# Performance work log

Hardware: AMD Instinct MI355X
Metric: run time of the kernel (lower is better)

Reference implementation:

```python
import jax, jax.numpy as jnp
import numpy as np

D_IN = 1024
D_OUT = 1024
SEQ = 2048
BATCH = 4


def setup_inputs() -> dict:
    key = jax.random.key(0)
    kx, kq, kk, kv = jax.random.split(key, 4)
    x = jax.random.normal(kx, (BATCH, SEQ, D_IN), dtype=jnp.float32)
    s = 1.0 / np.sqrt(D_IN)
    Wq = jax.random.uniform(kq, (D_IN, D_OUT), dtype=jnp.float32, minval=-s, maxval=s)
    Wk = jax.random.uniform(kk, (D_IN, D_OUT), dtype=jnp.float32, minval=-s, maxval=s)
    Wv = jax.random.uniform(kv, (D_IN, D_OUT), dtype=jnp.float32, minval=-s, maxval=s)
    return {"x": x, "Wq": Wq, "Wk": Wk, "Wv": Wv}


def reference(x, Wq, Wk, Wv):
    d_k = Wq.shape[1]
    q = jnp.einsum('bsd,de->bse', x, Wq)
    k = jnp.einsum('bsd,de->bse', x, Wk)
    v = jnp.einsum('bsd,de->bse', x, Wv)
    # [B, S, S] raw scores
    scores = jnp.einsum('bqe,bke->bqk', q, k)
    S = scores.shape[-1]
    causal = jnp.triu(jnp.ones((S, S), dtype=bool), k=1)  # True above diagonal
    scores = jnp.where(causal, -jnp.inf, scores)
    attn = jax.nn.softmax(scores * (d_k ** -0.5), axis=-1)
    # dropout p=0.0 -> identity
    return jnp.einsum('bqk,bke->bqe', attn, v)
```

## Files before the change

kernel.cpp:

```cpp
#include <hip/hip_runtime.h>
#include <hip/hip_bf16.h>

typedef unsigned short u16;
typedef __bf16 bfx8 __attribute__((ext_vector_type(8)));
typedef float fx4 __attribute__((ext_vector_type(4)));

#define SEQ 2048
#define DIM 1024
#define NBATCH 4
#define SCALE 0.03125f
#define NEL ((size_t)NBATCH * SEQ * DIM)

__device__ inline u16 f2bf(float f) {
    __bf16 h = (__bf16)f;
    return __builtin_bit_cast(unsigned short, h);
}

#define GLL(gp, lp) __builtin_amdgcn_global_load_lds( \
    (const __attribute__((address_space(1))) unsigned int*)(gp), \
    (__attribute__((address_space(3))) unsigned int*)(lp), 16, 0, 0)

__global__ __launch_bounds__(256) void prep(
    const float* __restrict__ X,
    const float* __restrict__ Wq, const float* __restrict__ Wk,
    const float* __restrict__ Wv,
    u16* __restrict__ XB, u16* __restrict__ WB, u16* __restrict__ WTv,
    float* __restrict__ Lrow)
{
    __shared__ u16 t[32][33];
    int bid = blockIdx.x;
    int tid = threadIdx.x;
    if (bid < 8192) {
        size_t i = (size_t)bid * 256 + tid;
        float4 v = ((const float4*)X)[i];
        uint2 pk;
        pk.x = (unsigned)f2bf(v.x) | ((unsigned)f2bf(v.y) << 16);
        pk.y = (unsigned)f2bf(v.z) | ((unsigned)f2bf(v.w) << 16);
        ((uint2*)XB)[i] = pk;
    } else if (bid < 10240) {
        int b2 = bid - 8192;
        const float* W = (b2 < 1024) ? Wq : Wk;
        u16* out = WB + (size_t)(b2 >> 10) * 1024 * 1024;
        size_t i = (size_t)(b2 & 1023) * 256 + tid;
        float4 v = ((const float4*)W)[i];
        uint2 pk;
        pk.x = (unsigned)f2bf(v.x) | ((unsigned)f2bf(v.y) << 16);
        pk.y = (unsigned)f2bf(v.z) | ((unsigned)f2bf(v.w) << 16);
        ((uint2*)out)[i] = pk;
    } else if (bid < 11264) {
        int t2 = bid - 10240;
        int n0 = (t2 & 31) * 32, k0 = (t2 >> 5) * 32;
        int tx = tid & 31, ty = tid >> 5;
        #pragma unroll
        for (int i = 0; i < 32; i += 8)
            t[ty + i][tx] = f2bf(Wv[(size_t)(k0 + ty + i) * 1024 + n0 + tx]);
        __syncthreads();
        #pragma unroll
        for (int i = 0; i < 32; i += 8)
            WTv[(size_t)(n0 + ty + i) * 1024 + k0 + tx] = t[tx][ty + i];
    } else {
        int i = (bid - 11264) * 256 + tid;
        Lrow[i] = 0.0f;
    }
}

__global__ __launch_bounds__(256) void gemm_m(
    const u16* __restrict__ WBk, const u16* __restrict__ WBq, u16* __restrict__ MT)
{
    int m0 = blockIdx.y * 128, n0 = blockIdx.x * 128;
    __shared__ __align__(16) u16 As[128 * 32];
    __shared__ __align__(16) u16 Bs[128 * 32];
    int tid = threadIdx.x, lane = tid & 63, w = tid >> 6;
    int wm = w >> 1, wn = w & 1, lo = lane & 15, qd = lane >> 4;
    fx4 acc[4][4] = {};

    int c0 = tid, c1 = tid + 256;
    const u16* a0 = WBk + (size_t)(m0 + (c0 >> 2)) * 1024 + (((c0 & 3) ^ ((c0 >> 2) & 3)) * 8);
    const u16* a1 = WBk + (size_t)(m0 + (c1 >> 2)) * 1024 + (((c1 & 3) ^ ((c1 >> 2) & 3)) * 8);
    const u16* b0 = WBq + (size_t)(n0 + (c0 >> 2)) * 1024 + (((c0 & 3) ^ ((c0 >> 2) & 3)) * 8);
    const u16* b1 = WBq + (size_t)(n0 + (c1 >> 2)) * 1024 + (((c1 & 3) ^ ((c1 >> 2) & 3)) * 8);

    int sw = (qd ^ (lo & 3)) * 8;
    for (int k0 = 0; k0 < 1024; k0 += 32) {
        GLL(a0 + k0, &As[(size_t)c0 * 8]);
        GLL(a1 + k0, &As[(size_t)c1 * 8]);
        GLL(b0 + k0, &Bs[(size_t)c0 * 8]);
        GLL(b1 + k0, &Bs[(size_t)c1 * 8]);
        __syncthreads();
        bfx8 af[4], bf[4];
        #pragma unroll
        for (int i = 0; i < 4; i++)
            af[i] = *(const bfx8*)(&As[(wm * 64 + i * 16 + lo) * 32 + sw]);
        #pragma unroll
        for (int j = 0; j < 4; j++)
            bf[j] = *(const bfx8*)(&Bs[(wn * 64 + j * 16 + lo) * 32 + sw]);
        #pragma unroll
        for (int i = 0; i < 4; i++)
            #pragma unroll
            for (int j = 0; j < 4; j++)
                acc[i][j] = __builtin_amdgcn_mfma_f32_16x16x32_bf16(af[i], bf[j], acc[i][j], 0, 0, 0);
        __syncthreads();
    }
    #pragma unroll
    for (int i = 0; i < 4; i++)
        #pragma unroll
        for (int j = 0; j < 4; j++)
            #pragma unroll
            for (int r = 0; r < 4; r++)
                MT[(size_t)(m0 + wm * 64 + i * 16 + qd * 4 + r) * 1024
                   + n0 + wn * 64 + j * 16 + lo] = f2bf(acc[i][j][r]);
}

__global__ __launch_bounds__(512) void gemm256(
    const u16* __restrict__ XB, const u16* __restrict__ MT,
    const u16* __restrict__ WTv,
    u16* __restrict__ Yo, u16* __restrict__ VTo)
{
    const int work = ((blockIdx.x & 7) << 5) + ((int)blockIdx.x >> 3);
    const int z = work >> 7;
    const int m0 = ((work >> 2) & 31) * 256;
    const int n0 = (work & 3) * 256;
    const u16* Bop = (z == 0) ? MT : WTv;

    __shared__ __align__(16) u16 SM[65536];

    const int tid = threadIdx.x, lane = tid & 63, w = tid >> 6;
    const int wm = w >> 2, wn = w & 3, lo = lane & 15, qd = lane >> 4;
    const int swl = lo & 7;

    fx4 acc[8][4] = {};

    const u16* sA[4]; const u16* sB[4]; int dofs[4];
    #pragma unroll
    for (int p = 0; p < 4; ++p) {
        int n = p * 512 + tid;
        int row = n >> 3;
        int c = (n & 7) ^ (row & 7);
        sA[p] = XB  + (size_t)(m0 + row) * 1024 + c * 8;
        sB[p] = Bop + (size_t)(n0 + row) * 1024 + c * 8;
        dofs[p] = n * 8;
    }

    auto stage = [&](int kt2) {
        const int bb = (kt2 & 1) * 16384;
        #pragma unroll
        for (int p = 0; p < 4; ++p) GLL(sA[p] + kt2 * 64, &SM[bb + dofs[p]]);
        #pragma unroll
        for (int p = 0; p < 4; ++p) GLL(sB[p] + kt2 * 64, &SM[32768 + bb + dofs[p]]);
    };

    stage(0);
    stage(1);
    asm volatile("s_waitcnt vmcnt(8)" ::: "memory");
    __builtin_amdgcn_s_barrier();
    asm volatile("" ::: "memory");

    bfx8 af[4][2], bfA[2][2], bfB[2][2];

    for (int kt = 0; kt < 16; ++kt) {
        const u16* Ab = SM + (kt & 1) * 16384;
        const u16* Bb = SM + 32768 + (kt & 1) * 16384;

        #pragma unroll
        for (int ph = 0; ph < 4; ++ph) {
            const int mh = ph >> 1, nh = ph & 1;
            if (nh == 0) {
                #pragma unroll
                for (int ii = 0; ii < 4; ++ii)
                    #pragma unroll
                    for (int ks = 0; ks < 2; ++ks)
                        af[ii][ks] = *(const bfx8*)(Ab
                            + (wm * 128 + (mh * 4 + ii) * 16 + lo) * 64
                            + ((ks * 4 + qd) ^ swl) * 8);
            }
            if (ph == 0) {
                #pragma unroll
                for (int jn = 0; jn < 2; ++jn)
                    #pragma unroll
                    for (int ks = 0; ks < 2; ++ks)
                        bfA[jn][ks] = *(const bfx8*)(Bb
                            + (wn * 64 + jn * 16 + lo) * 64
                            + ((ks * 4 + qd) ^ swl) * 8);
            }
            if (ph == 1) {
                #pragma unroll
                for (int jn = 0; jn < 2; ++jn)
                    #pragma unroll
                    for (int ks = 0; ks < 2; ++ks)
                        bfB[jn][ks] = *(const bfx8*)(Bb
                            + (wn * 64 + (2 + jn) * 16 + lo) * 64
                            + ((ks * 4 + qd) ^ swl) * 8);
            }
            __builtin_amdgcn_s_barrier();
            asm volatile("s_waitcnt lgkmcnt(0)" ::: "memory");
            __builtin_amdgcn_sched_barrier(0);
            __builtin_amdgcn_s_setprio(1);
            #pragma unroll
            for (int ii = 0; ii < 4; ++ii)
                #pragma unroll
                for (int jn = 0; jn < 2; ++jn)
                    #pragma unroll
                    for (int ks = 0; ks < 2; ++ks) {
                        if (nh == 0)
                            acc[mh * 4 + ii][jn] = __builtin_amdgcn_mfma_f32_16x16x32_bf16(
                                af[ii][ks], bfA[jn][ks], acc[mh * 4 + ii][jn], 0, 0, 0);
                        else
                            acc[mh * 4 + ii][2 + jn] = __builtin_amdgcn_mfma_f32_16x16x32_bf16(
                                af[ii][ks], bfB[jn][ks], acc[mh * 4 + ii][2 + jn], 0, 0, 0);
                    }
            __builtin_amdgcn_s_setprio(0);
            __builtin_amdgcn_s_barrier();
            asm volatile("" ::: "memory");
        }
        if (kt < 14) stage(kt + 2);
        if (kt < 15) {
            if (kt < 14) asm volatile("s_waitcnt vmcnt(8)" ::: "memory");
            else         asm volatile("s_waitcnt vmcnt(0)" ::: "memory");
            __builtin_amdgcn_s_barrier();
            asm volatile("" ::: "memory");
        }
    }

    if (z == 0) {
        #pragma unroll
        for (int i = 0; i < 8; i++)
            #pragma unroll
            for (int j = 0; j < 4; j++)
                #pragma unroll
                for (int r = 0; r < 4; r++) {
                    int row = m0 + wm * 128 + i * 16 + qd * 4 + r;
                    int col = n0 + wn * 64 + j * 16 + lo;
                    Yo[(size_t)row * 1024 + col] = f2bf(acc[i][j][r]);
                }
    } else {
        u16 (*Ct)[258] = (u16(*)[258])SM;
        const int bb = m0 >> 11;
        const int sbase = m0 & 2047;
        #pragma unroll
        for (int half = 0; half < 2; ++half) {
            __syncthreads();
            if (wm == half) {
                #pragma unroll
                for (int i = 0; i < 8; i++)
                    #pragma unroll
                    for (int j = 0; j < 4; j++)
                        #pragma unroll
                        for (int r = 0; r < 4; r++)
                            Ct[i * 16 + qd * 4 + r][wn * 64 + j * 16 + lo] = f2bf(acc[i][j][r]);
            }
            __syncthreads();
            for (int e = tid; e < 16384; e += 512) {
                int d = e >> 6, s2 = (e & 63) * 2;
                unsigned pk = (unsigned)Ct[s2][d] | ((unsigned)Ct[s2 + 1][d] << 16);
                *(unsigned*)&VTo[((size_t)bb * DIM + (n0 + d)) * SEQ
                                 + sbase + half * 128 + s2] = pk;
            }
        }
    }
}

__global__ __launch_bounds__(512) void sgemm_exp(
    const u16* __restrict__ Y, const u16* __restrict__ XB,
    u16* __restrict__ P, float* __restrict__ Lrow)
{
    const int k = blockIdx.x;
    const int work = (k & 7) * 68 + (k >> 3);
    const int b = work / 136;
    const int t = work % 136;
    int i = (int)((sqrtf(8.0f * t + 1.0f) - 1.0f) * 0.5f);
    while ((i + 1) * (i + 2) / 2 <= t) i++;
    while (i * (i + 1) / 2 > t) i--;
    int j = t - i * (i + 1) / 2;

    const u16* Yb = Y + (size_t)b * SEQ * DIM;
    const u16* Xb = XB + (size_t)b * SEQ * DIM;
    u16* Pb = P + (size_t)b * SEQ * SEQ;
    float* Lb = Lrow + (size_t)b * SEQ;

    int m0 = i * 128, n0 = j * 128;

    __shared__ __align__(16) u16 SM[32768];

    int tid = threadIdx.x, lane = tid & 63, w = tid >> 6;
    int wm = w >> 2, wn = w & 3, lo = lane & 15, qd = lane >> 4;
    int swl = lo & 7;

    fx4 acc[4][2] = {};

    int c0 = tid, c1 = tid + 512;
    const u16* a0 = Yb + (size_t)(m0 + (c0 >> 3)) * 1024 + (((c0 & 7) ^ ((c0 >> 3) & 7)) * 8);
    const u16* a1 = Yb + (size_t)(m0 + (c1 >> 3)) * 1024 + (((c1 & 7) ^ ((c1 >> 3) & 7)) * 8);
    const u16* b0 = Xb + (size_t)(n0 + (c0 >> 3)) * 1024 + (((c0 & 7) ^ ((c0 >> 3) & 7)) * 8);
    const u16* b1 = Xb + (size_t)(n0 + (c1 >> 3)) * 1024 + (((c1 & 7) ^ ((c1 >> 3) & 7)) * 8);
    int d0 = c0 * 8, d1 = c1 * 8;

    auto stage = [&](int kt2) {
        int bb = (kt2 & 1) * 8192;
        GLL(a0 + kt2 * 64, &SM[bb + d0]);
        GLL(a1 + kt2 * 64, &SM[bb + d1]);
        GLL(b0 + kt2 * 64, &SM[16384 + bb + d0]);
        GLL(b1 + kt2 * 64, &SM[16384 + bb + d1]);
    };

    stage(0);
    stage(1);
    asm volatile("s_waitcnt vmcnt(4)" ::: "memory");
    __builtin_amdgcn_s_barrier();
    asm volatile("" ::: "memory");

    for (int kt = 0; kt < 16; ++kt) {
        const u16* Ab = SM + (kt & 1) * 8192;
        const u16* Bb = SM + 16384 + (kt & 1) * 8192;

        #pragma unroll
        for (int kc = 0; kc < 2; ++kc) {
            bfx8 af[4], bf[2];
            int sw = ((kc * 4 + qd) ^ swl) * 8;
            #pragma unroll
            for (int ii = 0; ii < 4; ++ii)
                af[ii] = *(const bfx8*)(Ab + (wm * 64 + ii * 16 + lo) * 64 + sw);
            #pragma unroll
            for (int jn = 0; jn < 2; ++jn)
                bf[jn] = *(const bfx8*)(Bb + (wn * 32 + jn * 16 + lo) * 64 + sw);
            __builtin_amdgcn_s_barrier();
            asm volatile("s_waitcnt lgkmcnt(0)" ::: "memory");
            __builtin_amdgcn_sched_barrier(0);
            __builtin_amdgcn_s_setprio(1);
            #pragma unroll
            for (int ii = 0; ii < 4; ++ii)
                #pragma unroll
                for (int jn = 0; jn < 2; ++jn)
                    acc[ii][jn] = __builtin_amdgcn_mfma_f32_16x16x32_bf16(af[ii], bf[jn], acc[ii][jn], 0, 0, 0);
            __builtin_amdgcn_s_setprio(0);
            __builtin_amdgcn_s_barrier();
            asm volatile("" ::: "memory");
        }
        if (kt < 14) stage(kt + 2);
        if (kt < 15) {
            if (kt < 14) asm volatile("s_waitcnt vmcnt(4)" ::: "memory");
            else         asm volatile("s_waitcnt vmcnt(0)" ::: "memory");
            __builtin_amdgcn_s_barrier();
            asm volatile("" ::: "memory");
        }
    }

    #pragma unroll
    for (int ii = 0; ii < 4; ii++)
        #pragma unroll
        for (int r = 0; r < 4; r++) {
            int row = m0 + wm * 64 + ii * 16 + qd * 4 + r;
            float rs = 0.0f;
            #pragma unroll
            for (int jn = 0; jn < 2; jn++) {
                int col = n0 + wn * 32 + jn * 16 + lo;
                float s = acc[ii][jn][r] * SCALE;
                s = fminf(fmaxf(s, -30.0f), 30.0f);
                float p = (col > row) ? 0.0f : __expf(s);
                Pb[(size_t)row * SEQ + col] = f2bf(p);
                rs += p;
            }
            #pragma unroll
            for (int off = 1; off < 16; off <<= 1) rs += __shfl_xor(rs, off);
            if (lo == 0) atomicAdd(&Lb[row], rs);
        }
}

__global__ __launch_bounds__(512) void pvgemm(
    const u16* __restrict__ P, const u16* __restrict__ VT,
    const float* __restrict__ Lrow, float* __restrict__ O)
{
    const int k = blockIdx.x;
    const int xcd = k & 7, slot = k >> 3;
    const int b = xcd >> 1, half = xcd & 1;
    const int qsel = slot >> 3, db = slot & 7;
    const int qb = half ? (11 - qsel)
                        : ((qsel < 4) ? (15 - qsel) : (7 - qsel));
    int m0 = qb * 128, n0 = db * 128;
    int nkt = (qb + 1) * 2;

    const u16* Pb = P + (size_t)b * SEQ * SEQ;
    const u16* Vb = VT + (size_t)b * DIM * SEQ;
    const float* Lb = Lrow + (size_t)b * SEQ;
    float* Ob = O + (size_t)b * SEQ * DIM;

    __shared__ __align__(16) u16 SM[32768];

    int tid = threadIdx.x, lane = tid & 63, w = tid >> 6;
    int wm = w >> 2, wn = w & 3, lo = lane & 15, qd = lane >> 4;
    int swl = lo & 7;

    fx4 acc[4][2] = {};

    int c0 = tid, c1 = tid + 512;
    const u16* a0 = Pb + (size_t)(m0 + (c0 >> 3)) * SEQ + (((c0 & 7) ^ ((c0 >> 3) & 7)) * 8);
    const u16* a1 = Pb + (size_t)(m0 + (c1 >> 3)) * SEQ + (((c1 & 7) ^ ((c1 >> 3) & 7)) * 8);
    const u16* b0 = Vb + (size_t)(n0 + (c0 >> 3)) * SEQ + (((c0 & 7) ^ ((c0 >> 3) & 7)) * 8);
    const u16* b1 = Vb + (size_t)(n0 + (c1 >> 3)) * SEQ + (((c1 & 7) ^ ((c1 >> 3) & 7)) * 8);
    int d0 = c0 * 8, d1 = c1 * 8;

    auto stage = [&](int kt2) {
        int bb = (kt2 & 1) * 8192;
        GLL(a0 + kt2 * 64, &SM[bb + d0]);
        GLL(a1 + kt2 * 64, &SM[bb + d1]);
        GLL(b0 + kt2 * 64, &SM[16384 + bb + d0]);
        GLL(b1 + kt2 * 64, &SM[16384 + bb + d1]);
    };

    stage(0);
    stage(1);
    asm volatile("s_waitcnt vmcnt(4)" ::: "memory");
    __builtin_amdgcn_s_barrier();
    asm volatile("" ::: "memory");

    for (int kt = 0; kt < nkt; ++kt) {
        const u16* Ab = SM + (kt & 1) * 8192;
        const u16* Bb = SM + 16384 + (kt & 1) * 8192;

        #pragma unroll
        for (int kc = 0; kc < 2; ++kc) {
            bfx8 af[4], bf[2];
            int sw = ((kc * 4 + qd) ^ swl) * 8;
            #pragma unroll
            for (int ii = 0; ii < 4; ++ii)
                af[ii] = *(const bfx8*)(Ab + (wm * 64 + ii * 16 + lo) * 64 + sw);
            #pragma unroll
            for (int jn = 0; jn < 2; ++jn)
                bf[jn] = *(const bfx8*)(Bb + (wn * 32 + jn * 16 + lo) * 64 + sw);
            __builtin_amdgcn_s_barrier();
            asm volatile("s_waitcnt lgkmcnt(0)" ::: "memory");
            __builtin_amdgcn_sched_barrier(0);
            __builtin_amdgcn_s_setprio(1);
            #pragma unroll
            for (int ii = 0; ii < 4; ++ii)
                #pragma unroll
                for (int jn = 0; jn < 2; ++jn)
                    acc[ii][jn] = __builtin_amdgcn_mfma_f32_16x16x32_bf16(af[ii], bf[jn], acc[ii][jn], 0, 0, 0);
            __builtin_amdgcn_s_setprio(0);
            __builtin_amdgcn_s_barrier();
            asm volatile("" ::: "memory");
        }
        if (kt + 2 < nkt) stage(kt + 2);
        if (kt + 1 < nkt) {
            if (kt + 2 < nkt) asm volatile("s_waitcnt vmcnt(4)" ::: "memory");
            else              asm volatile("s_waitcnt vmcnt(0)" ::: "memory");
            __builtin_amdgcn_s_barrier();
            asm volatile("" ::: "memory");
        }
    }

    #pragma unroll
    for (int ii = 0; ii < 4; ii++)
        #pragma unroll
        for (int r = 0; r < 4; r++) {
            int row = m0 + wm * 64 + ii * 16 + qd * 4 + r;
            float linv = 1.0f / Lb[row];
            #pragma unroll
            for (int jn = 0; jn < 2; jn++) {
                int col = n0 + wn * 32 + jn * 16 + lo;
                Ob[(size_t)row * DIM + col] = acc[ii][jn][r] * linv;
            }
        }
}

__global__ __launch_bounds__(256) void gemm_legacy(
    const float* __restrict__ X,
    const float* __restrict__ Wq, const float* __restrict__ Wk, const float* __restrict__ Wv,
    u16* __restrict__ Qo, u16* __restrict__ Ko, u16* __restrict__ VTo)
{
    const int K = 1024, N = 1024;
    const float* W = (blockIdx.z == 0) ? Wq : (blockIdx.z == 1) ? Wk : Wv;
    int m0 = blockIdx.y * 128, n0 = blockIdx.x * 128;
    __shared__ __align__(16) u16 As[128 * 40];
    __shared__ __align__(16) u16 Bs[128 * 40];
    __shared__ __align__(16) u16 Ct[64][132];
    int tid = threadIdx.x, lane = tid & 63, w = tid >> 6;
    int wm = w >> 1, wn = w & 1, lo = lane & 15, qd = lane >> 4;
    fx4 acc[4][4] = {};
    for (int k0 = 0; k0 < K; k0 += 32) {
        #pragma unroll
        for (int c = tid; c < 1024; c += 256) {
            int row = c >> 3, cc = (c & 7) * 4;
            float4 v = *(const float4*)(X + (size_t)(m0 + row) * K + k0 + cc);
            uint2 pk;
            pk.x = (unsigned)f2bf(v.x) | ((unsigned)f2bf(v.y) << 16);
            pk.y = (unsigned)f2bf(v.z) | ((unsigned)f2bf(v.w) << 16);
            *(uint2*)(&As[row * 40 + cc]) = pk;
        }
        #pragma unroll
        for (int c = tid; c < 1024; c += 256) {
            int r = c >> 5, cc = (c & 31) * 4;
            float4 v = *(const float4*)(W + (size_t)(k0 + r) * N + n0 + cc);
            Bs[(cc + 0) * 40 + r] = f2bf(v.x);
            Bs[(cc + 1) * 40 + r] = f2bf(v.y);
            Bs[(cc + 2) * 40 + r] = f2bf(v.z);
            Bs[(cc + 3) * 40 + r] = f2bf(v.w);
        }
        __syncthreads();
        bfx8 af[4], bf[4];
        #pragma unroll
        for (int i = 0; i < 4; i++)
            af[i] = *(const bfx8*)(&As[(wm * 64 + i * 16 + lo) * 40 + qd * 8]);
        #pragma unroll
        for (int j = 0; j < 4; j++)
            bf[j] = *(const bfx8*)(&Bs[(wn * 64 + j * 16 + lo) * 40 + qd * 8]);
        #pragma unroll
        for (int i = 0; i < 4; i++)
            #pragma unroll
            for (int j = 0; j < 4; j++)
                acc[i][j] = __builtin_amdgcn_mfma_f32_16x16x32_bf16(af[i], bf[j], acc[i][j], 0, 0, 0);
        __syncthreads();
    }
    if (blockIdx.z != 2) {
        u16* C = (blockIdx.z == 0) ? Qo : Ko;
        #pragma unroll
        for (int i = 0; i < 4; i++)
            #pragma unroll
            for (int j = 0; j < 4; j++)
                #pragma unroll
                for (int r = 0; r < 4; r++) {
                    int row = m0 + wm * 64 + i * 16 + qd * 4 + r;
                    int col = n0 + wn * 64 + j * 16 + lo;
                    C[(size_t)row * N + col] = f2bf(acc[i][j][r]);
                }
    } else {
        #pragma unroll
        for (int half = 0; half < 2; half++) {
            __syncthreads();
            if (wm == half) {
                #pragma unroll
                for (int i = 0; i < 4; i++)
                    #pragma unroll
                    for (int j = 0; j < 4; j++)
                        #pragma unroll
                        for (int r = 0; r < 4; r++)
                            Ct[i * 16 + qd * 4 + r][wn * 64 + j * 16 + lo] = f2bf(acc[i][j][r]);
            }
            __syncthreads();
            #pragma unroll
            for (int e = tid; e < 64 * 128; e += 256) {
                int d = e >> 6, sl = e & 63;
                int gr = m0 + half * 64 + sl;
                int bb = gr >> 11, s = gr & 2047;
                VTo[((size_t)bb * DIM + (n0 + d)) * SEQ + s] = Ct[sl][d];
            }
        }
    }
}

__global__ __launch_bounds__(512) void flash_attn(
    const u16* __restrict__ Q, const u16* __restrict__ Kmat,
    const u16* __restrict__ VT, float* __restrict__ O)
{
    int b = blockIdx.y;
    int qt = (int)(gridDim.x - 1) - (int)blockIdx.x;
    int q0 = qt * 32;
    int tid = threadIdx.x;
    int lane = tid & 63, w = tid >> 6;
    int lo = lane & 15, qd = lane >> 4;

    __shared__ __align__(16) float Sp[8][32][33];
    __shared__ __align__(16) __bf16 Pl[32][40];
    __shared__ float ml[32], ll[32], al[32];

    const u16* Qb = Q + (size_t)b * SEQ * DIM;
    const u16* Kb = Kmat + (size_t)b * SEQ * DIM;
    const u16* VTb = VT + (size_t)b * DIM * SEQ;

    bfx8 qf[2][4];
    #pragma unroll
    for (int i = 0; i < 2; i++)
        #pragma unroll
        for (int c = 0; c < 4; c++)
            qf[i][c] = *(const bfx8*)(Qb + (size_t)(q0 + i * 16 + lo) * DIM + w * 128 + c * 32 + qd * 8);

    fx4 oacc[2][8] = {};
    if (tid < 32) { ml[tid] = -INFINITY; ll[tid] = 0.0f; }
    __syncthreads();

    for (int kt = 0; kt <= qt; kt++) {
        int k0 = kt * 32;
        fx4 sp[2][2] = {};
        #pragma unroll
        for (int c = 0; c < 4; c++) {
            bfx8 kf[2];
            #pragma unroll
            for (int jn = 0; jn < 2; jn++)
                kf[jn] = *(const bfx8*)(Kb + (size_t)(k0 + jn * 16 + lo) * DIM + w * 128 + c * 32 + qd * 8);
            #pragma unroll
            for (int i = 0; i < 2; i++)
                #pragma unroll
                for (int jn = 0; jn < 2; jn++)
                    sp[i][jn] = __builtin_amdgcn_mfma_f32_16x16x32_bf16(qf[i][c], kf[jn], sp[i][jn], 0, 0, 0);
        }
        #pragma unroll
        for (int i = 0; i < 2; i++)
            #pragma unroll
            for (int jn = 0; jn < 2; jn++)
                #pragma unroll
                for (int r = 0; r < 4; r++)
                    Sp[w][i * 16 + qd * 4 + r][jn * 16 + lo] = sp[i][jn][r];
        __syncthreads();
        {
            int r = tid >> 4, ci = tid & 15;
            int q = q0 + r;
            float s0 = 0.0f, s1 = 0.0f;
            #pragma unroll
            for (int p = 0; p < 8; p++) { s0 += Sp[p][r][ci]; s1 += Sp[p][r][ci + 16]; }
            s0 = fminf(fmaxf(s0 * SCALE, -1e30f), 1e30f);
            s1 = fminf(fmaxf(s1 * SCALE, -1e30f), 1e30f);
            if (k0 + ci > q)      s0 = -INFINITY;
            if (k0 + ci + 16 > q) s1 = -INFINITY;
            float mx = fmaxf(s0, s1);
            #pragma unroll
            for (int off = 1; off < 16; off <<= 1) mx = fmaxf(mx, __shfl_xor(mx, off));
            float mo = ml[r];
            float mn = fmaxf(mo, mx);
            float p0 = __expf(s0 - mn), p1 = __expf(s1 - mn);
            Pl[r][ci] = (__bf16)p0;
            Pl[r][ci + 16] = (__bf16)p1;
            float ps = p0 + p1;
            #pragma unroll
            for (int off = 1; off < 16; off <<= 1) ps += __shfl_xor(ps, off);
            if (ci == 0) {
                float alpha = __expf(mo - mn);
                ll[r] = alpha * ll[r] + ps;
                ml[r] = mn;
                al[r] = alpha;
            }
        }
        __syncthreads();
        float alocal[2][4];
        #pragma unroll
        for (int i = 0; i < 2; i++)
            #pragma unroll
            for (int r = 0; r < 4; r++)
                alocal[i][r] = al[i * 16 + qd * 4 + r];
        #pragma unroll
        for (int i = 0; i < 2; i++)
            #pragma unroll
            for (int j = 0; j < 8; j++)
                #pragma unroll
                for (int r = 0; r < 4; r++)
                    oacc[i][j][r] *= alocal[i][r];
        bfx8 pf[2];
        #pragma unroll
        for (int i = 0; i < 2; i++)
            pf[i] = *(const bfx8*)(&Pl[i * 16 + lo][qd * 8]);
        #pragma unroll
        for (int j = 0; j < 8; j++) {
            bfx8 vf = *(const bfx8*)(VTb + (size_t)(w * 128 + j * 16 + lo) * SEQ + k0 + qd * 8);
            #pragma unroll
            for (int i = 0; i < 2; i++)
                oacc[i][j] = __builtin_amdgcn_mfma_f32_16x16x32_bf16(pf[i], vf, oacc[i][j], 0, 0, 0);
        }
    }

    float linv[2][4];
    #pragma unroll
    for (int i = 0; i < 2; i++)
        #pragma unroll
        for (int r = 0; r < 4; r++)
            linv[i][r] = 1.0f / ll[i * 16 + qd * 4 + r];
    float* Ob = O + (size_t)b * SEQ * DIM;
    #pragma unroll
    for (int i = 0; i < 2; i++)
        #pragma unroll
        for (int j = 0; j < 8; j++)
            #pragma unroll
            for (int r = 0; r < 4; r++) {
                int row = q0 + i * 16 + qd * 4 + r;
                int col = w * 128 + j * 16 + lo;
                Ob[(size_t)row * DIM + col] = oacc[i][j][r] * linv[i][r];
            }
}

extern "C" void kernel_launch(void* const* d_in, const int* in_sizes, int n_in,
                              void* d_out, int out_size, void* d_ws, size_t ws_size,
                              hipStream_t stream) {
    const float* x  = (const float*)d_in[0];
    const float* Wq = (const float*)d_in[1];
    const float* Wk = (const float*)d_in[2];
    const float* Wv = (const float*)d_in[3];

    u16* ws = (u16*)d_ws;
    u16* Yp  = ws;
    u16* VTp = ws + NEL;
    u16* XBp = ws + 2 * NEL;
    u16* WBp = ws + 3 * NEL;
    u16* WTv = WBp + (size_t)2 * 1024 * 1024;
    u16* MTp = WTv + (size_t)1024 * 1024;
    u16* Pm  = MTp + (size_t)1024 * 1024;
    float* Lrow = (float*)(Pm + (size_t)NBATCH * SEQ * SEQ);

    size_t need_mat = ((size_t)3 * NEL + (size_t)4 * 1024 * 1024
                     + (size_t)NBATCH * SEQ * SEQ) * 2
                     + (size_t)NBATCH * SEQ * 4 + 1024;

    if (ws_size >= need_mat) {
        prep<<<dim3(11296), 256, 0, stream>>>(x, Wq, Wk, Wv, XBp, WBp, WTv, Lrow);
        gemm_m<<<dim3(8, 8), 256, 0, stream>>>(
            WBp + (size_t)1024 * 1024 , WBp , MTp);
        gemm256<<<dim3(256), 512, 0, stream>>>(XBp, MTp, WTv, Yp, VTp);
        sgemm_exp<<<dim3(544), 512, 0, stream>>>(Yp, XBp, Pm, Lrow);
        pvgemm<<<dim3(512), 512, 0, stream>>>(Pm, VTp, Lrow, (float*)d_out);
    } else {
        u16* Qp = ws; u16* Kp = ws + NEL; u16* VTf = ws + 2 * NEL;
        gemm_legacy<<<dim3(8, 64, 3), 256, 0, stream>>>(x, Wq, Wk, Wv, Qp, Kp, VTf);
        flash_attn<<<dim3(SEQ / 32, NBATCH), 512, 0, stream>>>(
            Qp, Kp, VTf, (float*)d_out);
    }
}
```

Measured before the change: 215.9 us.

## Split gemm256 tile across 16 waves with 64x64 per-wave subtiles

Doubles the gemm256 block from 512 to 1024 threads so each wave owns a 64x64 output subtile instead of 128x64. The per-wave accumulators halve, and the four-phase fragment reloads are replaced by a simple two-step k loop. Global-to-LDS staging and the V-transpose epilogue are spread over the larger block. The intent is more resident waves per CU to hide LDS and MFMA latency. The trade-off is that each wave loads more LDS data per MFMA. The launch bound `(1024, 4)` requests a high minimum occupancy, which may cap VGPRs tightly enough to cause spills.

```diff
diff --git a/kernel.cpp b/kernel.cpp
--- a/kernel.cpp
+++ b/kernel.cpp
@@ -111,7 +111,7 @@
                    + n0 + wn * 64 + j * 16 + lo] = f2bf(acc[i][j][r]);
 }
 
-__global__ __launch_bounds__(512) void gemm256(
+__global__ __launch_bounds__(1024, 4) void gemm256(
     const u16* __restrict__ XB, const u16* __restrict__ MT,
     const u16* __restrict__ WTv,
     u16* __restrict__ Yo, u16* __restrict__ VTo)
@@ -128,12 +128,12 @@
     const int wm = w >> 2, wn = w & 3, lo = lane & 15, qd = lane >> 4;
     const int swl = lo & 7;
 
-    fx4 acc[8][4] = {};
-
-    const u16* sA[4]; const u16* sB[4]; int dofs[4];
+    fx4 acc[4][4] = {};
+
+    const u16* sA[2]; const u16* sB[2]; int dofs[2];
     #pragma unroll
-    for (int p = 0; p < 4; ++p) {
-        int n = p * 512 + tid;
+    for (int p = 0; p < 2; ++p) {
+        int n = p * 1024 + tid;
         int row = n >> 3;
         int c = (n & 7) ^ (row & 7);
         sA[p] = XB  + (size_t)(m0 + row) * 1024 + c * 8;
@@ -144,77 +144,48 @@
     auto stage = [&](int kt2) {
         const int bb = (kt2 & 1) * 16384;
         #pragma unroll
-        for (int p = 0; p < 4; ++p) GLL(sA[p] + kt2 * 64, &SM[bb + dofs[p]]);
-        #pragma unroll
-        for (int p = 0; p < 4; ++p) GLL(sB[p] + kt2 * 64, &SM[32768 + bb + dofs[p]]);
+        for (int p = 0; p < 2; ++p) GLL(sA[p] + kt2 * 64, &SM[bb + dofs[p]]);
+        #pragma unroll
+        for (int p = 0; p < 2; ++p) GLL(sB[p] + kt2 * 64, &SM[32768 + bb + dofs[p]]);
     };
 
     stage(0);
     stage(1);
-    asm volatile("s_waitcnt vmcnt(8)" ::: "memory");
+    asm volatile("s_waitcnt vmcnt(4)" ::: "memory");
     __builtin_amdgcn_s_barrier();
     asm volatile("" ::: "memory");
-
-    bfx8 af[4][2], bfA[2][2], bfB[2][2];
 
     for (int kt = 0; kt < 16; ++kt) {
         const u16* Ab = SM + (kt & 1) * 16384;
         const u16* Bb = SM + 32768 + (kt & 1) * 16384;
 
         #pragma unroll
-        for (int ph = 0; ph < 4; ++ph) {
-            const int mh = ph >> 1, nh = ph & 1;
-            if (nh == 0) {
-                #pragma unroll
-                for (int ii = 0; ii < 4; ++ii)
-                    #pragma unroll
-                    for (int ks = 0; ks < 2; ++ks)
-                        af[ii][ks] = *(const bfx8*)(Ab
-                            + (wm * 128 + (mh * 4 + ii) * 16 + lo) * 64
-                            + ((ks * 4 + qd) ^ swl) * 8);
-            }
-            if (ph == 0) {
-                #pragma unroll
-                for (int jn = 0; jn < 2; ++jn)
-                    #pragma unroll
-                    for (int ks = 0; ks < 2; ++ks)
-                        bfA[jn][ks] = *(const bfx8*)(Bb
-                            + (wn * 64 + jn * 16 + lo) * 64
-                            + ((ks * 4 + qd) ^ swl) * 8);
-            }
-            if (ph == 1) {
-                #pragma unroll
-                for (int jn = 0; jn < 2; ++jn)
-                    #pragma unroll
-                    for (int ks = 0; ks < 2; ++ks)
-                        bfB[jn][ks] = *(const bfx8*)(Bb
-                            + (wn * 64 + (2 + jn) * 16 + lo) * 64
-                            + ((ks * 4 + qd) ^ swl) * 8);
-            }
+        for (int ks = 0; ks < 2; ++ks) {
+            bfx8 af[4], bf[4];
+            const int sw = ((ks * 4 + qd) ^ swl) * 8;
+            #pragma unroll
+            for (int i = 0; i < 4; ++i)
+                af[i] = *(const bfx8*)(Ab + (wm * 64 + i * 16 + lo) * 64 + sw);
+            #pragma unroll
+            for (int j = 0; j < 4; ++j)
+                bf[j] = *(const bfx8*)(Bb + (wn * 64 + j * 16 + lo) * 64 + sw);
             __builtin_amdgcn_s_barrier();
             asm volatile("s_waitcnt lgkmcnt(0)" ::: "memory");
             __builtin_amdgcn_sched_barrier(0);
             __builtin_amdgcn_s_setprio(1);
             #pragma unroll
-            for (int ii = 0; ii < 4; ++ii)
-                #pragma unroll
-                for (int jn = 0; jn < 2; ++jn)
-                    #pragma unroll
-                    for (int ks = 0; ks < 2; ++ks) {
-                        if (nh == 0)
-                            acc[mh * 4 + ii][jn] = __builtin_amdgcn_mfma_f32_16x16x32_bf16(
-                                af[ii][ks], bfA[jn][ks], acc[mh * 4 + ii][jn], 0, 0, 0);
-                        else
-                            acc[mh * 4 + ii][2 + jn] = __builtin_amdgcn_mfma_f32_16x16x32_bf16(
-                                af[ii][ks], bfB[jn][ks], acc[mh * 4 + ii][2 + jn], 0, 0, 0);
-                    }
+            for (int i = 0; i < 4; ++i)
+                #pragma unroll
+                for (int j = 0; j < 4; ++j)
+                    acc[i][j] = __builtin_amdgcn_mfma_f32_16x16x32_bf16(
+                        af[i], bf[j], acc[i][j], 0, 0, 0);
             __builtin_amdgcn_s_setprio(0);
             __builtin_amdgcn_s_barrier();
             asm volatile("" ::: "memory");
         }
         if (kt < 14) stage(kt + 2);
         if (kt < 15) {
-            if (kt < 14) asm volatile("s_waitcnt vmcnt(8)" ::: "memory");
+            if (kt < 14) asm volatile("s_waitcnt vmcnt(4)" ::: "memory");
             else         asm volatile("s_waitcnt vmcnt(0)" ::: "memory");
             __builtin_amdgcn_s_barrier();
             asm volatile("" ::: "memory");
@@ -223,12 +194,12 @@
 
     if (z == 0) {
         #pragma unroll
-        for (int i = 0; i < 8; i++)
+        for (int i = 0; i < 4; i++)
             #pragma unroll
             for (int j = 0; j < 4; j++)
                 #pragma unroll
                 for (int r = 0; r < 4; r++) {
-                    int row = m0 + wm * 128 + i * 16 + qd * 4 + r;
+                    int row = m0 + wm * 64 + i * 16 + qd * 4 + r;
                     int col = n0 + wn * 64 + j * 16 + lo;
                     Yo[(size_t)row * 1024 + col] = f2bf(acc[i][j][r]);
                 }
@@ -237,23 +208,24 @@
         const int bb = m0 >> 11;
         const int sbase = m0 & 2047;
         #pragma unroll
-        for (int half = 0; half < 2; ++half) {
+        for (int h = 0; h < 2; ++h) {
             __syncthreads();
-            if (wm == half) {
-                #pragma unroll
-                for (int i = 0; i < 8; i++)
+            if ((wm >> 1) == h) {
+                #pragma unroll
+                for (int i = 0; i < 4; i++)
                     #pragma unroll
                     for (int j = 0; j < 4; j++)
                         #pragma unroll
                         for (int r = 0; r < 4; r++)
-                            Ct[i * 16 + qd * 4 + r][wn * 64 + j * 16 + lo] = f2bf(acc[i][j][r]);
+                            Ct[(wm & 1) * 64 + i * 16 + qd * 4 + r]
+                              [wn * 64 + j * 16 + lo] = f2bf(acc[i][j][r]);
             }
             __syncthreads();
-            for (int e = tid; e < 16384; e += 512) {
+            for (int e = tid; e < 16384; e += 1024) {
                 int d = e >> 6, s2 = (e & 63) * 2;
                 unsigned pk = (unsigned)Ct[s2][d] | ((unsigned)Ct[s2 + 1][d] << 16);
                 *(unsigned*)&VTo[((size_t)bb * DIM + (n0 + d)) * SEQ
-                                 + sbase + half * 128 + s2] = pk;
+                                 + sbase + h * 128 + s2] = pk;
             }
         }
     }
@@ -700,7 +672,7 @@
         prep<<<dim3(11296), 256, 0, stream>>>(x, Wq, Wk, Wv, XBp, WBp, WTv, Lrow);
         gemm_m<<<dim3(8, 8), 256, 0, stream>>>(
             WBp + (size_t)1024 * 1024 , WBp , MTp);
-        gemm256<<<dim3(256), 512, 0, stream>>>(XBp, MTp, WTv, Yp, VTp);
+        gemm256<<<dim3(256), 1024, 0, stream>>>(XBp, MTp, WTv, Yp, VTp);
         sgemm_exp<<<dim3(544), 512, 0, stream>>>(Yp, XBp, Pm, Lrow);
         pvgemm<<<dim3(512), 512, 0, stream>>>(Pm, VTp, Lrow, (float*)d_out);
     } else {
```

After: 217.1 us. No clear change (+0.6%).

## Split global-to-LDS staging into half-tiles interleaved with MFMA phases

Applied to the files above, without the earlier changes.

The projection GEMM used to issue all next-tile global_load_lds copies in one burst after the compute phases. It now splits A and B staging into 128-row halves, issues each half between the four MFMA phases, and adjusts the vmcnt waits to match. The aim is to overlap global memory traffic with matrix math and smooth memory-issue bursts. The cost is more complex synchronization, and there is a risk of LDS hazards if any half is overwritten while other waves are still reading it.

```diff
diff --git a/kernel.cpp b/kernel.cpp
--- a/kernel.cpp
+++ b/kernel.cpp
@@ -130,91 +130,137 @@
 
     fx4 acc[8][4] = {};
 
-    const u16* sA[4]; const u16* sB[4]; int dofs[4];
+    const u16* sA[2][2]; const u16* sB[2][2]; int dofs[2][2];
     #pragma unroll
-    for (int p = 0; p < 4; ++p) {
-        int n = p * 512 + tid;
-        int row = n >> 3;
-        int c = (n & 7) ^ (row & 7);
-        sA[p] = XB  + (size_t)(m0 + row) * 1024 + c * 8;
-        sB[p] = Bop + (size_t)(n0 + row) * 1024 + c * 8;
-        dofs[p] = n * 8;
-    }
-
-    auto stage = [&](int kt2) {
+    for (int h = 0; h < 2; ++h)
+        #pragma unroll
+        for (int p = 0; p < 2; ++p) {
+            int n = p * 512 + tid;
+            int rl = n >> 3;
+            int c = (n & 7) ^ (rl & 7);
+            sA[h][p] = XB  + (size_t)(m0 + h * 128 + rl) * 1024 + c * 8;
+            sB[h][p] = Bop + (size_t)(n0 + h * 128 + rl) * 1024 + c * 8;
+            dofs[h][p] = (h * 1024 + n) * 8;
+        }
+
+    auto stageA = [&](int kt2, int h) {
         const int bb = (kt2 & 1) * 16384;
-        #pragma unroll
-        for (int p = 0; p < 4; ++p) GLL(sA[p] + kt2 * 64, &SM[bb + dofs[p]]);
-        #pragma unroll
-        for (int p = 0; p < 4; ++p) GLL(sB[p] + kt2 * 64, &SM[32768 + bb + dofs[p]]);
+        GLL(sA[h][0] + kt2 * 64, &SM[bb + dofs[h][0]]);
+        GLL(sA[h][1] + kt2 * 64, &SM[bb + dofs[h][1]]);
     };
-
-    stage(0);
-    stage(1);
-    asm volatile("s_waitcnt vmcnt(8)" ::: "memory");
+    auto stageB = [&](int kt2, int h) {
+        const int bb = 32768 + (kt2 & 1) * 16384;
+        GLL(sB[h][0] + kt2 * 64, &SM[bb + dofs[h][0]]);
+        GLL(sB[h][1] + kt2 * 64, &SM[bb + dofs[h][1]]);
+    };
+
+    stageA(0, 0); stageA(0, 1); stageB(0, 0); stageB(0, 1);
+    stageA(1, 0); stageB(1, 0);
+    asm volatile("s_waitcnt vmcnt(4)" ::: "memory");
     __builtin_amdgcn_s_barrier();
     asm volatile("" ::: "memory");
 
-    bfx8 af[4][2], bfA[2][2], bfB[2][2];
-
+    #pragma unroll 2
     for (int kt = 0; kt < 16; ++kt) {
         const u16* Ab = SM + (kt & 1) * 16384;
         const u16* Bb = SM + 32768 + (kt & 1) * 16384;
 
-        #pragma unroll
-        for (int ph = 0; ph < 4; ++ph) {
-            const int mh = ph >> 1, nh = ph & 1;
-            if (nh == 0) {
-                #pragma unroll
-                for (int ii = 0; ii < 4; ++ii)
-                    #pragma unroll
-                    for (int ks = 0; ks < 2; ++ks)
-                        af[ii][ks] = *(const bfx8*)(Ab
-                            + (wm * 128 + (mh * 4 + ii) * 16 + lo) * 64
-                            + ((ks * 4 + qd) ^ swl) * 8);
-            }
-            if (ph == 0) {
-                #pragma unroll
-                for (int jn = 0; jn < 2; ++jn)
-                    #pragma unroll
-                    for (int ks = 0; ks < 2; ++ks)
-                        bfA[jn][ks] = *(const bfx8*)(Bb
-                            + (wn * 64 + jn * 16 + lo) * 64
-                            + ((ks * 4 + qd) ^ swl) * 8);
-            }
-            if (ph == 1) {
-                #pragma unroll
-                for (int jn = 0; jn < 2; ++jn)
-                    #pragma unroll
-                    for (int ks = 0; ks < 2; ++ks)
-                        bfB[jn][ks] = *(const bfx8*)(Bb
-                            + (wn * 64 + (2 + jn) * 16 + lo) * 64
-                            + ((ks * 4 + qd) ^ swl) * 8);
-            }
-            __builtin_amdgcn_s_barrier();
-            asm volatile("s_waitcnt lgkmcnt(0)" ::: "memory");
-            __builtin_amdgcn_sched_barrier(0);
-            __builtin_amdgcn_s_setprio(1);
-            #pragma unroll
-            for (int ii = 0; ii < 4; ++ii)
-                #pragma unroll
-                for (int jn = 0; jn < 2; ++jn)
-                    #pragma unroll
-                    for (int ks = 0; ks < 2; ++ks) {
-                        if (nh == 0)
-                            acc[mh * 4 + ii][jn] = __builtin_amdgcn_mfma_f32_16x16x32_bf16(
-                                af[ii][ks], bfA[jn][ks], acc[mh * 4 + ii][jn], 0, 0, 0);
-                        else
-                            acc[mh * 4 + ii][2 + jn] = __builtin_amdgcn_mfma_f32_16x16x32_bf16(
-                                af[ii][ks], bfB[jn][ks], acc[mh * 4 + ii][2 + jn], 0, 0, 0);
-                    }
-            __builtin_amdgcn_s_setprio(0);
-            __builtin_amdgcn_s_barrier();
-            asm volatile("" ::: "memory");
-        }
-        if (kt < 14) stage(kt + 2);
+        bfx8 af[4][2], b0r[2][2], b1r[2][2];
+
+        #pragma unroll
+        for (int ii = 0; ii < 4; ++ii)
+            #pragma unroll
+            for (int ks = 0; ks < 2; ++ks)
+                af[ii][ks] = *(const bfx8*)(Ab + (wm * 128 + ii * 16 + lo) * 64
+                                            + ((ks * 4 + qd) ^ swl) * 8);
+        #pragma unroll
+        for (int jn = 0; jn < 2; ++jn)
+            #pragma unroll
+            for (int ks = 0; ks < 2; ++ks)
+                b0r[jn][ks] = *(const bfx8*)(Bb + (wn * 64 + jn * 16 + lo) * 64
+                                             + ((ks * 4 + qd) ^ swl) * 8);
+        if (kt < 15) stageA(kt + 1, 1);
+        asm volatile("s_waitcnt lgkmcnt(8)" ::: "memory");
+        __builtin_amdgcn_s_barrier();
+        asm volatile("s_waitcnt lgkmcnt(0)" ::: "memory");
+        __builtin_amdgcn_sched_barrier(0);
+        __builtin_amdgcn_s_setprio(1);
+        #pragma unroll
+        for (int ii = 0; ii < 4; ++ii)
+            #pragma unroll
+            for (int jn = 0; jn < 2; ++jn)
+                #pragma unroll
+                for (int ks = 0; ks < 2; ++ks)
+                    acc[ii][jn] = __builtin_amdgcn_mfma_f32_16x16x32_bf16(
+                        af[ii][ks], b0r[jn][ks], acc[ii][jn], 0, 0, 0);
+        __builtin_amdgcn_s_setprio(0);
+        __builtin_amdgcn_s_barrier();
+        asm volatile("" ::: "memory");
+
+        #pragma unroll
+        for (int jn = 0; jn < 2; ++jn)
+            #pragma unroll
+            for (int ks = 0; ks < 2; ++ks)
+                b1r[jn][ks] = *(const bfx8*)(Bb + (wn * 64 + (2 + jn) * 16 + lo) * 64
+                                             + ((ks * 4 + qd) ^ swl) * 8);
+        if (kt < 15) stageB(kt + 1, 1);
+        __builtin_amdgcn_s_barrier();
+        asm volatile("s_waitcnt lgkmcnt(0)" ::: "memory");
+        __builtin_amdgcn_sched_barrier(0);
+        __builtin_amdgcn_s_setprio(1);
+        #pragma unroll
+        for (int ii = 0; ii < 4; ++ii)
+            #pragma unroll
+            for (int jn = 0; jn < 2; ++jn)
+                #pragma unroll
+                for (int ks = 0; ks < 2; ++ks)
+                    acc[ii][2 + jn] = __builtin_amdgcn_mfma_f32_16x16x32_bf16(
+                        af[ii][ks], b1r[jn][ks], acc[ii][2 + jn], 0, 0, 0);
+        __builtin_amdgcn_s_setprio(0);
+        __builtin_amdgcn_s_barrier();
+        asm volatile("" ::: "memory");
+
+        #pragma unroll
+        for (int ii = 0; ii < 4; ++ii)
+            #pragma unroll
+            for (int ks = 0; ks < 2; ++ks)
+                af[ii][ks] = *(const bfx8*)(Ab + (wm * 128 + (4 + ii) * 16 + lo) * 64
+                                            + ((ks * 4 + qd) ^ swl) * 8);
+        if (kt < 14) stageA(kt + 2, 0);
+        __builtin_amdgcn_s_barrier();
+        asm volatile("s_waitcnt lgkmcnt(0)" ::: "memory");
+        __builtin_amdgcn_sched_barrier(0);
+        __builtin_amdgcn_s_setprio(1);
+        #pragma unroll
+        for (int ii = 0; ii < 4; ++ii)
+            #pragma unroll
+            for (int jn = 0; jn < 2; ++jn)
+                #pragma unroll
+                for (int ks = 0; ks < 2; ++ks)
+                    acc[4 + ii][jn] = __builtin_amdgcn_mfma_f32_16x16x32_bf16(
+                        af[ii][ks], b0r[jn][ks], acc[4 + ii][jn], 0, 0, 0);
+        __builtin_amdgcn_s_setprio(0);
+        __builtin_amdgcn_s_barrier();
+        asm volatile("" ::: "memory");
+
+        if (kt < 14) stageB(kt + 2, 0);
+        __builtin_amdgcn_s_barrier();
+        __builtin_amdgcn_sched_barrier(0);
+        __builtin_amdgcn_s_setprio(1);
+        #pragma unroll
+        for (int ii = 0; ii < 4; ++ii)
+            #pragma unroll
+            for (int jn = 0; jn < 2; ++jn)
+                #pragma unroll
+                for (int ks = 0; ks < 2; ++ks)
+                    acc[4 + ii][2 + jn] = __builtin_amdgcn_mfma_f32_16x16x32_bf16(
+                        af[ii][ks], b1r[jn][ks], acc[4 + ii][2 + jn], 0, 0, 0);
+        __builtin_amdgcn_s_setprio(0);
+        __builtin_amdgcn_s_barrier();
+        asm volatile("" ::: "memory");
+
         if (kt < 15) {
-            if (kt < 14) asm volatile("s_waitcnt vmcnt(8)" ::: "memory");
+            if (kt < 14) asm volatile("s_waitcnt vmcnt(4)" ::: "memory");
             else         asm volatile("s_waitcnt vmcnt(0)" ::: "memory");
             __builtin_amdgcn_s_barrier();
             asm volatile("" ::: "memory");
```

Measured after the change: 208.7 us, median of 3. -3.3%, faster.
